# Optimization experiments

Measured on AMD Instinct MI355X. Metric: run time of the kernel, lower is better.

## Reference

```python
import jax, jax.numpy as jnp
import numpy as np

B, T, D_MODEL, D_HIDDEN, MAX_SEQLEN = 4, 2048, 1024, 1024, 2048


def setup_inputs() -> dict:
    key = jax.random.key(0)
    ks = jax.random.split(key, 8)
    scale = 0.02  # keep exp() and linear outputs in a sane range
    return {
        "q": jax.random.normal(ks[0], (B, T, D_MODEL), dtype=jnp.float32),
        "k": jax.random.normal(ks[1], (B, T, D_MODEL), dtype=jnp.float32),
        "v": jax.random.normal(ks[2], (B, T, D_MODEL), dtype=jnp.float32),
        "Wq": jax.random.normal(ks[3], (D_HIDDEN, D_MODEL), dtype=jnp.float32) * scale,
        "Wk": jax.random.normal(ks[4], (D_HIDDEN, D_MODEL), dtype=jnp.float32) * scale,
        "Wv": jax.random.normal(ks[5], (D_HIDDEN, D_MODEL), dtype=jnp.float32) * scale,
        "Wo": jax.random.normal(ks[6], (D_MODEL, D_HIDDEN), dtype=jnp.float32) * scale,
        "W_bias": jax.random.normal(ks[7], (MAX_SEQLEN, MAX_SEQLEN), dtype=jnp.float32) * scale,
    }


def reference(q, k, v, Wq, Wk, Wv, Wo, W_bias):
    Ti = q.shape[1]
    Tj = k.shape[1]
    # Linear projections (torch Linear: x @ W.T), bias=False
    Q = jnp.einsum('btm,hm->bth', q, Wq)
    K = jnp.einsum('btm,hm->bth', k, Wk)
    V = jnp.einsum('btm,hm->bth', v, Wv)
    pos_bias = W_bias[:Ti, :Tj][None]              # (1, Ti, Tj)
    # Faithful to original: max over dim 0 (batch dim for K, singleton dim for pos_bias)
    max_key = jnp.max(K, axis=0, keepdims=True)    # (1, Tj, Dh)
    max_pos_bias = jnp.max(pos_bias, axis=0, keepdims=True)  # == pos_bias (dim 0 is size 1)
    exp_key = jnp.exp(K - max_key)                 # (B, Tj, Dh)
    exp_pos_bias = jnp.exp(pos_bias - max_pos_bias)  # all-ones, kept for faithfulness
    num = jnp.einsum('bij,bjd->bid', exp_pos_bias, exp_key * V)
    den = jnp.einsum('bij,bjd->bid', exp_pos_bias, exp_key)
    Yt = jax.nn.sigmoid(Q) * num / den             # (B, Ti, Dh)
    return jnp.einsum('bth,mh->btm', Yt, Wo)
```

## Files before the change

kernel.cpp:

```cpp
#include <hip/hip_runtime.h>
#include <hip/hip_bf16.h>

typedef __bf16 bf16;
typedef __bf16 bf16x8 __attribute__((ext_vector_type(8)));
typedef __bf16 bf16x4 __attribute__((ext_vector_type(4)));
typedef float f32x4 __attribute__((ext_vector_type(4)));

#define B_   4
#define T_   2048
#define DM_  1024
#define DH_  1024
#define MROWS 8192

struct CvtJob { const float* src; bf16* dst; int nf4; };
struct CvtArgs { CvtJob job[7]; };

__global__ __launch_bounds__(256) void cvt_kernel(CvtArgs args) {
  CvtJob jb = args.job[blockIdx.y];
  int base = blockIdx.x * 2048;
  if (base >= jb.nf4) return;
  int t2 = threadIdx.x * 2;
  const float4* s = (const float4*)jb.src;
  float4 a[4][2];
#pragma unroll
  for (int u = 0; u < 4; ++u) {
    a[u][0] = s[base + u * 512 + t2];
    a[u][1] = s[base + u * 512 + t2 + 1];
  }
#pragma unroll
  for (int u = 0; u < 4; ++u) {
    bf16x8 o;
    o[0] = (bf16)a[u][0].x; o[1] = (bf16)a[u][0].y;
    o[2] = (bf16)a[u][0].z; o[3] = (bf16)a[u][0].w;
    o[4] = (bf16)a[u][1].x; o[5] = (bf16)a[u][1].y;
    o[6] = (bf16)a[u][1].z; o[7] = (bf16)a[u][1].w;
    *(bf16x8*)(jb.dst + ((size_t)base + u * 512 + t2) * 4) = o;
  }
}

struct GemmJob { const bf16* A; const bf16* Bw; float* Cf; bf16* Cb; int mode; };
struct GemmArgs { GemmJob job[4]; int N; int K; };

__global__ __launch_bounds__(256) void gemm_bt(GemmArgs ga) {
  const GemmJob jb = ga.job[blockIdx.z];
  const int N = ga.N, K = ga.K;
  __shared__ bf16 As[128 * 64];
  __shared__ bf16 Bs[128 * 64];

  const int tid  = threadIdx.x;
  const int lane = tid & 63;
  const int wave = tid >> 6;
  const int wm   = (wave >> 1) * 64;
  const int wn   = (wave & 1) * 64;

  const int f   = blockIdx.y * 8 + blockIdx.x;
  const int xcd = f & 7;
  const int j   = f >> 3;
  const int bn  = j & 7;
  const int bm  = (j >> 3) * 8 + xcd;
  const int tileM = bm * 128;
  const int tileN = bn * 128;

  f32x4 acc[4][4] = {};

  const int sr = lane >> 3;
  const int sc = (lane & 7) ^ sr;

  for (int k0 = 0; k0 < K; k0 += 64) {
#pragma unroll
    for (int l = 0; l < 4; ++l) {
      int grp = wave * 4 + l;
      int row = grp * 8 + sr;
      const bf16* gaadr = jb.A + (size_t)(tileM + row) * K + k0 + sc * 8;
      __builtin_amdgcn_global_load_lds(
          (const __attribute__((address_space(1))) void*)gaadr,
          (__attribute__((address_space(3))) void*)&As[grp * 512], 16, 0, 0);
      const bf16* gbadr = jb.Bw + (size_t)(tileN + row) * K + k0 + sc * 8;
      __builtin_amdgcn_global_load_lds(
          (const __attribute__((address_space(1))) void*)gbadr,
          (__attribute__((address_space(3))) void*)&Bs[grp * 512], 16, 0, 0);
    }
    __syncthreads();

    const int quad = lane >> 4;
#pragma unroll
    for (int s = 0; s < 2; ++s) {
      bf16x8 af[4], bfr[4];
#pragma unroll
      for (int mt = 0; mt < 4; ++mt) {
        int row = wm + mt * 16 + (lane & 15);
        int chunk = (s * 4 + quad) ^ (row & 7);
        af[mt] = *(const bf16x8*)&As[row * 64 + chunk * 8];
      }
#pragma unroll
      for (int nt = 0; nt < 4; ++nt) {
        int row = wn + nt * 16 + (lane & 15);
        int chunk = (s * 4 + quad) ^ (row & 7);
        bfr[nt] = *(const bf16x8*)&Bs[row * 64 + chunk * 8];
      }
#pragma unroll
      for (int mt = 0; mt < 4; ++mt)
#pragma unroll
        for (int nt = 0; nt < 4; ++nt)
          acc[mt][nt] = __builtin_amdgcn_mfma_f32_16x16x32_bf16(
              af[mt], bfr[nt], acc[mt][nt], 0, 0, 0);
    }
    __syncthreads();
  }

  const int cn = lane & 15;
  const int cr = (lane >> 4) * 4;
  if (jb.mode == 0) {
#pragma unroll
    for (int mt = 0; mt < 4; ++mt)
#pragma unroll
      for (int nt = 0; nt < 4; ++nt)
#pragma unroll
        for (int r = 0; r < 4; ++r) {
          int row = tileM + wm + mt * 16 + cr + r;
          int col = tileN + wn + nt * 16 + cn;
          jb.Cf[(size_t)row * N + col] = acc[mt][nt][r];
        }
  } else if (jb.mode == 1) {
#pragma unroll
    for (int mt = 0; mt < 4; ++mt)
#pragma unroll
      for (int nt = 0; nt < 4; ++nt)
#pragma unroll
        for (int r = 0; r < 4; ++r) {
          int row = tileM + wm + mt * 16 + cr + r;
          int col = tileN + wn + nt * 16 + cn;
          jb.Cb[(size_t)row * N + col] =
              (bf16)(1.f / (1.f + __expf(-acc[mt][nt][r])));
        }
  } else {
#pragma unroll
    for (int mt = 0; mt < 4; ++mt)
#pragma unroll
      for (int nt = 0; nt < 4; ++nt)
#pragma unroll
        for (int r = 0; r < 4; ++r) {
          int row = tileM + wm + mt * 16 + cr + r;
          int col = tileN + wn + nt * 16 + cn;
          jb.Cb[(size_t)row * N + col] = (bf16)acc[mt][nt][r];
        }
  }
}

__global__ __launch_bounds__(256) void reduce_kv(
    const bf16* __restrict__ Kb, const bf16* __restrict__ Vb,
    float* __restrict__ part) {
  __shared__ float lds[64 * 128];
  const int t = threadIdx.x;
  const int half = t >> 7;
  const int dt = t & 127;
  const int d = dt * 8;
  const int j0 = blockIdx.x * 8 + half * 4;
  const size_t bs = (size_t)T_ * DH_;
  float n[4][8] = {}, e[4][8] = {};
  for (int jj = j0; jj < j0 + 4; ++jj) {
    size_t off = (size_t)jj * DH_ + d;
    bf16x8 kk[4], vv[4];
#pragma unroll
    for (int b = 0; b < 4; ++b) {
      kk[b] = *(const bf16x8*)(Kb + off + b * bs);
      vv[b] = *(const bf16x8*)(Vb + off + b * bs);
    }
#pragma unroll
    for (int c = 0; c < 8; ++c) {
      float k0 = (float)kk[0][c], k1 = (float)kk[1][c];
      float k2 = (float)kk[2][c], k3 = (float)kk[3][c];
      float m = fmaxf(fmaxf(k0, k1), fmaxf(k2, k3));
      float w0 = __expf(k0 - m), w1 = __expf(k1 - m);
      float w2 = __expf(k2 - m), w3 = __expf(k3 - m);
      e[0][c] += w0; e[1][c] += w1; e[2][c] += w2; e[3][c] += w3;
      n[0][c] += w0 * (float)vv[0][c];
      n[1][c] += w1 * (float)vv[1][c];
      n[2][c] += w2 * (float)vv[2][c];
      n[3][c] += w3 * (float)vv[3][c];
    }
  }
  if (half) {
#pragma unroll
    for (int b = 0; b < 4; ++b)
#pragma unroll
      for (int c = 0; c < 8; ++c) {
        lds[(b * 8 + c) * 128 + dt] = n[b][c];
        lds[(32 + b * 8 + c) * 128 + dt] = e[b][c];
      }
  }
  __syncthreads();
  if (!half) {
    float* po = part + (size_t)blockIdx.x * 8192;
#pragma unroll
    for (int b = 0; b < 4; ++b)
#pragma unroll
      for (int c = 0; c < 8; ++c) {
        po[b * 1024 + d + c] = n[b][c] + lds[(b * 8 + c) * 128 + dt];
        po[4096 + b * 1024 + d + c] = e[b][c] + lds[(32 + b * 8 + c) * 128 + dt];
      }
  }
}

__global__ __launch_bounds__(256) void finish_kv(
    const float* __restrict__ part, float* __restrict__ numden) {
  __shared__ float lds[128];
  const int t = threadIdx.x;
  const int half = t >> 7;
  const int sl = t & 127;
  const int slot = blockIdx.x * 128 + sl;
  float s = 0.f;
  for (int i = half * 128; i < half * 128 + 128; i += 8) {
#pragma unroll
    for (int u = 0; u < 8; ++u)
      s += part[(size_t)(i + u) * 8192 + slot];
  }
  if (half) lds[sl] = s;
  __syncthreads();
  if (!half) numden[slot] = s + lds[sl];
}

__global__ __launch_bounds__(256) void mul_ratio(
    bf16* __restrict__ Yb, const float* __restrict__ num,
    const float* __restrict__ den) {
  size_t i = ((size_t)blockIdx.x * 256 + threadIdx.x) * 8;
  int h = (int)(i & (DH_ - 1));
  int b = (int)(i >> 21);
  bf16x8 y = *(bf16x8*)(Yb + i);
  const float* nu = num + b * DH_ + h;
  const float* de = den + b * DH_ + h;
  float4 n0 = *(const float4*)nu;
  float4 n1 = *(const float4*)(nu + 4);
  float4 d0 = *(const float4*)de;
  float4 d1 = *(const float4*)(de + 4);
  bf16x8 o;
  o[0] = (bf16)((float)y[0] * n0.x / d0.x);
  o[1] = (bf16)((float)y[1] * n0.y / d0.y);
  o[2] = (bf16)((float)y[2] * n0.z / d0.z);
  o[3] = (bf16)((float)y[3] * n0.w / d0.w);
  o[4] = (bf16)((float)y[4] * n1.x / d1.x);
  o[5] = (bf16)((float)y[5] * n1.y / d1.y);
  o[6] = (bf16)((float)y[6] * n1.z / d1.z);
  o[7] = (bf16)((float)y[7] * n1.w / d1.w);
  *(bf16x8*)(Yb + i) = o;
}

extern "C" void kernel_launch(void* const* d_in, const int* in_sizes, int n_in,
                              void* d_out, int out_size, void* d_ws, size_t ws_size,
                              hipStream_t stream) {
  const float* q  = (const float*)d_in[0];
  const float* k  = (const float*)d_in[1];
  const float* v  = (const float*)d_in[2];
  const float* Wq = (const float*)d_in[3];
  const float* Wk = (const float*)d_in[4];
  const float* Wv = (const float*)d_in[5];
  const float* Wo = (const float*)d_in[6];
  float* out = (float*)d_out;

  char* ws = (char*)d_ws;
  size_t off = 0;
  auto alloc = [&](size_t bytes) {
    char* p = ws + off;
    off += (bytes + 255) & ~(size_t)255;
    return p;
  };
  const size_t actN = (size_t)MROWS * DM_;
  const size_t wN   = (size_t)DH_ * DM_;

  bf16* qb  = (bf16*)alloc(actN * 2);
  bf16* kb  = (bf16*)alloc(actN * 2);
  bf16* vb  = (bf16*)alloc(actN * 2);
  bf16* Wqb = (bf16*)alloc(wN * 2);
  bf16* Wkb = (bf16*)alloc(wN * 2);
  bf16* Wvb = (bf16*)alloc(wN * 2);
  bf16* Wob = (bf16*)alloc(wN * 2);
  bf16* Kb  = (bf16*)alloc(actN * 2);
  bf16* Vb  = (bf16*)alloc(actN * 2);
  bf16* Yb  = (bf16*)alloc(actN * 2);
  float* part = (float*)alloc((size_t)256 * 8192 * 4);
  float* numden = (float*)alloc(8192 * 4);
  float* num = numden;
  float* den = numden + 4096;

  CvtArgs ca;
  ca.job[0] = {q,  qb,  (int)(actN / 4)};
  ca.job[1] = {k,  kb,  (int)(actN / 4)};
  ca.job[2] = {v,  vb,  (int)(actN / 4)};
  ca.job[3] = {Wq, Wqb, (int)(wN / 4)};
  ca.job[4] = {Wk, Wkb, (int)(wN / 4)};
  ca.job[5] = {Wv, Wvb, (int)(wN / 4)};
  ca.job[6] = {Wo, Wob, (int)(wN / 4)};
  cvt_kernel<<<dim3(actN / 4 / 2048, 7), 256, 0, stream>>>(ca);

  GemmArgs g1;
  g1.N = DH_; g1.K = DM_;
  g1.job[0] = {kb, Wkb, nullptr, Kb, 2};
  g1.job[1] = {vb, Wvb, nullptr, Vb, 2};
  g1.job[2] = {qb, Wqb, nullptr, Yb, 1};
  g1.job[3] = {nullptr, nullptr, nullptr, nullptr, 0};
  gemm_bt<<<dim3(8, MROWS / 128, 3), 256, 0, stream>>>(g1);

  reduce_kv<<<dim3(256), 256, 0, stream>>>(Kb, Vb, part);
  finish_kv<<<dim3(64), 256, 0, stream>>>(part, numden);

  mul_ratio<<<dim3(actN / 8 / 256), 256, 0, stream>>>(Yb, num, den);

  GemmArgs g2;
  g2.N = DM_; g2.K = DH_;
  g2.job[0] = {Yb, Wob, out, nullptr, 0};
  g2.job[1] = g2.job[2] = g2.job[3] = {nullptr, nullptr, nullptr, nullptr, 0};
  gemm_bt<<<dim3(8, MROWS / 128, 1), 256, 0, stream>>>(g2);
}
```

Measured before the change: 279.1 us.

## Fuse fp32-to-bf16 activation conversion into the projection GEMM A-tile loads

Stops converting q, k and v to bf16 in a separate pass. A new projection GEMM loads fp32 A rows directly into registers, converts them to bf16, writes them to swizzled LDS, and prefetches the next K-slice in registers. Only the weights still go through the convert kernel. This removes a full read and write of three 8192x1024 activations, but the GEMM now reads twice the A bytes and does the A staging through VALU and registers instead of direct-to-LDS loads. A minor unroll pragma is also added to reduce_kv.

```diff
diff --git a/kernel.cpp b/kernel.cpp
--- a/kernel.cpp
+++ b/kernel.cpp
@@ -3,7 +3,6 @@
 
 typedef __bf16 bf16;
 typedef __bf16 bf16x8 __attribute__((ext_vector_type(8)));
-typedef __bf16 bf16x4 __attribute__((ext_vector_type(4)));
 typedef float f32x4 __attribute__((ext_vector_type(4)));
 
 #define B_   4
@@ -13,7 +12,7 @@
 #define MROWS 8192
 
 struct CvtJob { const float* src; bf16* dst; int nf4; };
-struct CvtArgs { CvtJob job[7]; };
+struct CvtArgs { CvtJob job[4]; };
 
 __global__ __launch_bounds__(256) void cvt_kernel(CvtArgs args) {
   CvtJob jb = args.job[blockIdx.y];
@@ -38,11 +37,134 @@
   }
 }
 
-struct GemmJob { const bf16* A; const bf16* Bw; float* Cf; bf16* Cb; int mode; };
-struct GemmArgs { GemmJob job[4]; int N; int K; };
+struct GemmF32Job { const float* A; const bf16* Bw; bf16* Cb; int mode; };
+struct GemmF32Args { GemmF32Job job[3]; };
+
+__global__ __launch_bounds__(256) void gemm_f32a(GemmF32Args ga) {
+  const GemmF32Job jb = ga.job[blockIdx.z];
+  const int N = DH_, K = DM_;
+  __shared__ bf16 As[128 * 64];
+  __shared__ bf16 Bs[128 * 64];
+
+  const int tid  = threadIdx.x;
+  const int lane = tid & 63;
+  const int wave = tid >> 6;
+  const int wm   = (wave >> 1) * 64;
+  const int wn   = (wave & 1) * 64;
+
+  const int f   = blockIdx.y * 8 + blockIdx.x;
+  const int xcd = f & 7;
+  const int j   = f >> 3;
+  const int bn  = j & 7;
+  const int bm  = (j >> 3) * 8 + xcd;
+  const int tileM = bm * 128;
+  const int tileN = bn * 128;
+
+  f32x4 acc[4][4] = {};
+
+  const int sr = lane >> 3;
+  const int sc = (lane & 7) ^ sr;
+
+  const float* Abase = jb.A + (size_t)(tileM + wave * 32 + sr) * K + sc * 8;
+
+  float4 av[4][2];
+#pragma unroll
+  for (int l = 0; l < 4; ++l) {
+    const float* p = Abase + (size_t)(l * 8) * K;
+    av[l][0] = *(const float4*)p;
+    av[l][1] = *(const float4*)(p + 4);
+  }
+
+  for (int i = 0; i < K / 64; ++i) {
+    const int k0 = i * 64;
+#pragma unroll
+    for (int l = 0; l < 4; ++l) {
+      int grp = wave * 4 + l;
+      int row = grp * 8 + sr;
+      const bf16* gbadr = jb.Bw + (size_t)(tileN + row) * K + k0 + sc * 8;
+      __builtin_amdgcn_global_load_lds(
+          (const __attribute__((address_space(1))) void*)gbadr,
+          (__attribute__((address_space(3))) void*)&Bs[grp * 512], 16, 0, 0);
+    }
+#pragma unroll
+    for (int l = 0; l < 4; ++l) {
+      bf16x8 w;
+      w[0] = (bf16)av[l][0].x; w[1] = (bf16)av[l][0].y;
+      w[2] = (bf16)av[l][0].z; w[3] = (bf16)av[l][0].w;
+      w[4] = (bf16)av[l][1].x; w[5] = (bf16)av[l][1].y;
+      w[6] = (bf16)av[l][1].z; w[7] = (bf16)av[l][1].w;
+      *(bf16x8*)&As[(wave * 4 + l) * 512 + lane * 8] = w;
+    }
+    __syncthreads();
+
+    if (i + 1 < K / 64) {
+#pragma unroll
+      for (int l = 0; l < 4; ++l) {
+        const float* p = Abase + (size_t)(l * 8) * K + k0 + 64;
+        av[l][0] = *(const float4*)p;
+        av[l][1] = *(const float4*)(p + 4);
+      }
+    }
+
+    const int quad = lane >> 4;
+#pragma unroll
+    for (int s = 0; s < 2; ++s) {
+      bf16x8 af[4], bfr[4];
+#pragma unroll
+      for (int mt = 0; mt < 4; ++mt) {
+        int row = wm + mt * 16 + (lane & 15);
+        int chunk = (s * 4 + quad) ^ (row & 7);
+        af[mt] = *(const bf16x8*)&As[row * 64 + chunk * 8];
+      }
+#pragma unroll
+      for (int nt = 0; nt < 4; ++nt) {
+        int row = wn + nt * 16 + (lane & 15);
+        int chunk = (s * 4 + quad) ^ (row & 7);
+        bfr[nt] = *(const bf16x8*)&Bs[row * 64 + chunk * 8];
+      }
+#pragma unroll
+      for (int mt = 0; mt < 4; ++mt)
+#pragma unroll
+        for (int nt = 0; nt < 4; ++nt)
+          acc[mt][nt] = __builtin_amdgcn_mfma_f32_16x16x32_bf16(
+              af[mt], bfr[nt], acc[mt][nt], 0, 0, 0);
+    }
+    __syncthreads();
+  }
+
+  const int cn = lane & 15;
+  const int cr = (lane >> 4) * 4;
+  if (jb.mode == 1) {
+#pragma unroll
+    for (int mt = 0; mt < 4; ++mt)
+#pragma unroll
+      for (int nt = 0; nt < 4; ++nt)
+#pragma unroll
+        for (int r = 0; r < 4; ++r) {
+          int row = tileM + wm + mt * 16 + cr + r;
+          int col = tileN + wn + nt * 16 + cn;
+          jb.Cb[(size_t)row * N + col] =
+              (bf16)(1.f / (1.f + __expf(-acc[mt][nt][r])));
+        }
+  } else {
+#pragma unroll
+    for (int mt = 0; mt < 4; ++mt)
+#pragma unroll
+      for (int nt = 0; nt < 4; ++nt)
+#pragma unroll
+        for (int r = 0; r < 4; ++r) {
+          int row = tileM + wm + mt * 16 + cr + r;
+          int col = tileN + wn + nt * 16 + cn;
+          jb.Cb[(size_t)row * N + col] = (bf16)acc[mt][nt][r];
+        }
+  }
+}
+
+struct GemmJob { const bf16* A; const bf16* Bw; float* Cf; };
+struct GemmArgs { GemmJob job[1]; int N; int K; };
 
 __global__ __launch_bounds__(256) void gemm_bt(GemmArgs ga) {
-  const GemmJob jb = ga.job[blockIdx.z];
+  const GemmJob jb = ga.job[0];
   const int N = ga.N, K = ga.K;
   __shared__ bf16 As[128 * 64];
   __shared__ bf16 Bs[128 * 64];
@@ -110,41 +232,16 @@
 
   const int cn = lane & 15;
   const int cr = (lane >> 4) * 4;
-  if (jb.mode == 0) {
-#pragma unroll
-    for (int mt = 0; mt < 4; ++mt)
-#pragma unroll
-      for (int nt = 0; nt < 4; ++nt)
-#pragma unroll
-        for (int r = 0; r < 4; ++r) {
-          int row = tileM + wm + mt * 16 + cr + r;
-          int col = tileN + wn + nt * 16 + cn;
-          jb.Cf[(size_t)row * N + col] = acc[mt][nt][r];
-        }
-  } else if (jb.mode == 1) {
-#pragma unroll
-    for (int mt = 0; mt < 4; ++mt)
-#pragma unroll
-      for (int nt = 0; nt < 4; ++nt)
-#pragma unroll
-        for (int r = 0; r < 4; ++r) {
-          int row = tileM + wm + mt * 16 + cr + r;
-          int col = tileN + wn + nt * 16 + cn;
-          jb.Cb[(size_t)row * N + col] =
-              (bf16)(1.f / (1.f + __expf(-acc[mt][nt][r])));
-        }
-  } else {
-#pragma unroll
-    for (int mt = 0; mt < 4; ++mt)
-#pragma unroll
-      for (int nt = 0; nt < 4; ++nt)
-#pragma unroll
-        for (int r = 0; r < 4; ++r) {
-          int row = tileM + wm + mt * 16 + cr + r;
-          int col = tileN + wn + nt * 16 + cn;
-          jb.Cb[(size_t)row * N + col] = (bf16)acc[mt][nt][r];
-        }
-  }
+#pragma unroll
+  for (int mt = 0; mt < 4; ++mt)
+#pragma unroll
+    for (int nt = 0; nt < 4; ++nt)
+#pragma unroll
+      for (int r = 0; r < 4; ++r) {
+        int row = tileM + wm + mt * 16 + cr + r;
+        int col = tileN + wn + nt * 16 + cn;
+        jb.Cf[(size_t)row * N + col] = acc[mt][nt][r];
+      }
 }
 
 __global__ __launch_bounds__(256) void reduce_kv(
@@ -158,6 +255,7 @@
   const int j0 = blockIdx.x * 8 + half * 4;
   const size_t bs = (size_t)T_ * DH_;
   float n[4][8] = {}, e[4][8] = {};
+#pragma unroll 2
   for (int jj = j0; jj < j0 + 4; ++jj) {
     size_t off = (size_t)jj * DH_ + d;
     bf16x8 kk[4], vv[4];
@@ -267,9 +365,6 @@
   const size_t actN = (size_t)MROWS * DM_;
   const size_t wN   = (size_t)DH_ * DM_;
 
-  bf16* qb  = (bf16*)alloc(actN * 2);
-  bf16* kb  = (bf16*)alloc(actN * 2);
-  bf16* vb  = (bf16*)alloc(actN * 2);
   bf16* Wqb = (bf16*)alloc(wN * 2);
   bf16* Wkb = (bf16*)alloc(wN * 2);
   bf16* Wvb = (bf16*)alloc(wN * 2);
@@ -283,22 +378,17 @@
   float* den = numden + 4096;
 
   CvtArgs ca;
-  ca.job[0] = {q,  qb,  (int)(actN / 4)};
-  ca.job[1] = {k,  kb,  (int)(actN / 4)};
-  ca.job[2] = {v,  vb,  (int)(actN / 4)};
-  ca.job[3] = {Wq, Wqb, (int)(wN / 4)};
-  ca.job[4] = {Wk, Wkb, (int)(wN / 4)};
-  ca.job[5] = {Wv, Wvb, (int)(wN / 4)};
-  ca.job[6] = {Wo, Wob, (int)(wN / 4)};
-  cvt_kernel<<<dim3(actN / 4 / 2048, 7), 256, 0, stream>>>(ca);
-
-  GemmArgs g1;
-  g1.N = DH_; g1.K = DM_;
-  g1.job[0] = {kb, Wkb, nullptr, Kb, 2};
-  g1.job[1] = {vb, Wvb, nullptr, Vb, 2};
-  g1.job[2] = {qb, Wqb, nullptr, Yb, 1};
-  g1.job[3] = {nullptr, nullptr, nullptr, nullptr, 0};
-  gemm_bt<<<dim3(8, MROWS / 128, 3), 256, 0, stream>>>(g1);
+  ca.job[0] = {Wq, Wqb, (int)(wN / 4)};
+  ca.job[1] = {Wk, Wkb, (int)(wN / 4)};
+  ca.job[2] = {Wv, Wvb, (int)(wN / 4)};
+  ca.job[3] = {Wo, Wob, (int)(wN / 4)};
+  cvt_kernel<<<dim3(wN / 4 / 2048, 4), 256, 0, stream>>>(ca);
+
+  GemmF32Args g1;
+  g1.job[0] = {k, Wkb, Kb, 2};
+  g1.job[1] = {v, Wvb, Vb, 2};
+  g1.job[2] = {q, Wqb, Yb, 1};
+  gemm_f32a<<<dim3(8, MROWS / 128, 3), 256, 0, stream>>>(g1);
 
   reduce_kv<<<dim3(256), 256, 0, stream>>>(Kb, Vb, part);
   finish_kv<<<dim3(64), 256, 0, stream>>>(part, numden);
@@ -307,7 +397,6 @@
 
   GemmArgs g2;
   g2.N = DM_; g2.K = DH_;
-  g2.job[0] = {Yb, Wob, out, nullptr, 0};
-  g2.job[1] = g2.job[2] = g2.job[3] = {nullptr, nullptr, nullptr, nullptr, 0};
+  g2.job[0] = {Yb, Wob, out};
   gemm_bt<<<dim3(8, MROWS / 128, 1), 256, 0, stream>>>(g2);
 }
```

Measured after the change: 318.4 us. 14.1% more time.
